# Kernel tuning notes

Hardware: AMD Instinct MI355X
Metric: run time of the kernel (lower is better)

Reference implementation:

```python
import jax, jax.numpy as jnp
import numpy as np

N_SPANS = 4096
EMB_DIM = 384
HEADS = 4
DECAY_LAMBDA = 5.0
THRESHOLD = 0.1
NEG_SLOPE = 0.2  # PyG GATConv default leaky_relu slope


def setup_inputs() -> dict:
    key = jax.random.key(0)
    k1, k2, k3, k4, k5, k6 = jax.random.split(key, 6)
    embeddings = jax.random.normal(k1, (N_SPANS, EMB_DIM), dtype=jnp.float32)
    span_positions = jnp.sort(
        jax.random.randint(k2, (N_SPANS, 2), 0, 100000), axis=1
    ).astype(jnp.int64)
    # GATConv params: lin (no bias), per-head attention vectors, output bias
    glorot = 1.0 / np.sqrt(EMB_DIM)
    W = jax.random.normal(k3, (EMB_DIM, HEADS, EMB_DIM), dtype=jnp.float32) * glorot
    att_src = jax.random.normal(k4, (HEADS, EMB_DIM), dtype=jnp.float32) * glorot
    att_dst = jax.random.normal(k5, (HEADS, EMB_DIM), dtype=jnp.float32) * glorot
    bias = jnp.zeros((EMB_DIM,), dtype=jnp.float32)
    return {
        "embeddings": embeddings,
        "span_positions": span_positions,
        "W": W,
        "att_src": att_src,
        "att_dst": att_dst,
        "bias": bias,
    }


def _adjacency_mask(embeddings):
    # A_ij = cos_sim(e_i, e_j) * exp(-|i - j| / lambda); edges where A > 0.1
    n = embeddings.shape[0]
    en = embeddings / jnp.linalg.norm(embeddings, axis=1, keepdims=True)
    cos_sim = en @ en.T  # [N, N]
    idx = jnp.arange(n, dtype=embeddings.dtype)
    decay = jnp.exp(-jnp.abs(idx[None, :] - idx[:, None]) / DECAY_LAMBDA)
    adj = cos_sim * decay
    # diagonal is 1.0 > threshold, so self-loops (required by GATConv) are present
    return adj > THRESHOLD  # symmetric mask: mask[i, j] == edge j -> i


def reference(embeddings, span_positions, W, att_src, att_dst, bias):
    mask = _adjacency_mask(embeddings)  # [N_dst, N_src]
    # GATConv(heads=4, concat=False): project, per-head additive attention
    x = jnp.einsum("nd,dhe->nhe", embeddings, W)  # [N, H, E]
    a_src = jnp.einsum("nhe,he->nh", x, att_src)  # [N, H]
    a_dst = jnp.einsum("nhe,he->nh", x, att_dst)  # [N, H]
    # logits[i, j, h] for edge j -> i
    logits = jax.nn.leaky_relu(a_dst[:, None, :] + a_src[None, :, :], NEG_SLOPE)
    logits = jnp.where(mask[:, :, None], logits, jnp.float32(-jnp.inf))
    alpha = jax.nn.softmax(logits, axis=1)  # softmax over incoming sources j
    out = jnp.einsum("ijh,jhe->ihe", alpha, x)  # [N, H, E]
    out = out.mean(axis=1) + bias  # concat=False -> mean over heads, then bias
    return out
```

## Files before the change

### kernel.cpp

```cpp
#include <hip/hip_runtime.h>
#include <hip/hip_bf16.h>
#include <math.h>

#define N_SPANS 4096
#define EMB 384
#define HEADS 4
#define HE (HEADS * EMB)
#define BAND 11
#define BW (2 * BAND + 1)

typedef short bf16x8 __attribute__((ext_vector_type(8)));
typedef float f32x4 __attribute__((ext_vector_type(4)));

__device__ __forceinline__ unsigned short f2bf(float f) {
    union { float f; unsigned u; } x; x.f = f;
    unsigned r = x.u + 0x7fffu + ((x.u >> 16) & 1u);
    return (unsigned short)(r >> 16);
}
__device__ __forceinline__ float bf2f(unsigned short u) {
    union { unsigned u; float f; } x; x.u = ((unsigned)u) << 16; return x.f;
}

__device__ __forceinline__ float wave_sum(float v) {
    #pragma unroll
    for (int off = 32; off; off >>= 1) v += __shfl_xor(v, off, 64);
    return v;
}
__device__ __forceinline__ float wave_max(float v) {
    #pragma unroll
    for (int off = 32; off; off >>= 1) v = fmaxf(v, __shfl_xor(v, off, 64));
    return v;
}

__device__ __forceinline__ void gl2lds16(const void* g, void* l) {
    __builtin_amdgcn_global_load_lds(
        (const __attribute__((address_space(1))) void*)(uintptr_t)g,
        (__attribute__((address_space(3))) void*)(unsigned)(uintptr_t)l,
        16, 0, 0);
}

__global__ __launch_bounds__(256) void prep(const float* __restrict__ E,
                                            const float* __restrict__ W,
                                            unsigned short* __restrict__ Ebf,
                                            unsigned short* __restrict__ Wt,
                                            float* __restrict__ invn,
                                            float* __restrict__ attacc) {
    __shared__ float tile[32][33];
    const int b = blockIdx.x;
    const int tid = threadIdx.x;
    if (b < 1024) {
        const int lane = tid & 63, w = tid >> 6;
        const int n = b * 4 + w;
        const float4* er = (const float4*)(E + n * EMB);
        unsigned short* orow = Ebf + n * EMB;
        float s = 0.f;
        float4 v0 = er[lane];
        s += v0.x * v0.x + v0.y * v0.y + v0.z * v0.z + v0.w * v0.w;
        ushort4 c0;
        c0.x = f2bf(v0.x); c0.y = f2bf(v0.y); c0.z = f2bf(v0.z); c0.w = f2bf(v0.w);
        ((ushort4*)orow)[lane] = c0;
        if (lane < 32) {
            float4 v1 = er[lane + 64];
            s += v1.x * v1.x + v1.y * v1.y + v1.z * v1.z + v1.w * v1.w;
            ushort4 c1;
            c1.x = f2bf(v1.x); c1.y = f2bf(v1.y); c1.z = f2bf(v1.z); c1.w = f2bf(v1.w);
            ((ushort4*)orow)[lane + 64] = c1;
        }
        s = wave_sum(s);
        if (lane == 0) invn[n] = 1.0f / sqrtf(s);
    } else if (b < 1600) {
        const int t = b - 1024;
        const int n0 = (t % 48) * 32;
        const int k0 = (t / 48) * 32;
        const int tx = tid & 31, ty = tid >> 5;
        #pragma unroll
        for (int q = 0; q < 4; ++q)
            tile[ty + q * 8][tx] = W[(k0 + ty + q * 8) * HE + n0 + tx];
        __syncthreads();
        #pragma unroll
        for (int q = 0; q < 4; ++q)
            Wt[(n0 + ty + q * 8) * EMB + k0 + tx] = f2bf(tile[tx][ty + q * 8]);
    } else {
        const int t = b - 1600;
        ((float4*)attacc)[t * 256 + tid] = make_float4(0.f, 0.f, 0.f, 0.f);
    }
}

__global__ __launch_bounds__(256) void gemm_attn(const unsigned short* __restrict__ Ebf,
                                                 const unsigned short* __restrict__ Wt,
                                                 const float* __restrict__ attS,
                                                 const float* __restrict__ attD,
                                                 unsigned short* __restrict__ Xb,
                                                 float* __restrict__ asrc,
                                                 float* __restrict__ adst) {
    __shared__ unsigned short As[128 * 32];
    __shared__ unsigned short Bs[128 * 32];
    const int tid = threadIdx.x;
    const int lane = tid & 63;
    const int wave = tid >> 6;
    const int m0 = blockIdx.y * 128;
    const int n0 = blockIdx.x * 128;
    const int wr = (wave >> 1) * 64;
    const int wc = (wave & 1) * 64;
    const int quad = lane >> 4;
    const int l16 = lane & 15;

    const char* Ab = (const char*)Ebf + (size_t)(m0 + wave * 32 + (lane >> 2)) * 768 + (lane & 3) * 16;
    const char* Bb = (const char*)Wt  + (size_t)(n0 + wave * 32 + (lane >> 2)) * 768 + (lane & 3) * 16;
    char* AsB = (char*)As + wave * 32 * 64;
    char* BsB = (char*)Bs + wave * 32 * 64;

    f32x4 acc[4][4];
    #pragma unroll
    for (int i = 0; i < 4; ++i)
        #pragma unroll
        for (int j = 0; j < 4; ++j) acc[i][j] = 0.f;

    for (int kt = 0; kt < 12; ++kt) {
        const int kb = kt * 64;
        __syncthreads();
        gl2lds16(Ab + kb,            AsB);
        gl2lds16(Ab + kb + 16 * 768, AsB + 16 * 64);
        gl2lds16(Bb + kb,            BsB);
        gl2lds16(Bb + kb + 16 * 768, BsB + 16 * 64);
        __syncthreads();

        bf16x8 af[4], bfr[4];
        #pragma unroll
        for (int t = 0; t < 4; ++t) {
            af[t]  = *(const bf16x8*)(&As[(wr + t * 16 + l16) * 32 + quad * 8]);
            bfr[t] = *(const bf16x8*)(&Bs[(wc + t * 16 + l16) * 32 + quad * 8]);
        }
        #pragma unroll
        for (int ti = 0; ti < 4; ++ti)
            #pragma unroll
            for (int tj = 0; tj < 4; ++tj)
                acc[ti][tj] = __builtin_amdgcn_mfma_f32_16x16x32_bf16(
                    af[ti], bfr[tj], acc[ti][tj], 0, 0, 0);
    }

    const int hblk = (n0 + wc) / EMB;
    float aS[4], aD[4];
    #pragma unroll
    for (int tj = 0; tj < 4; ++tj) {
        int col = n0 + wc + tj * 16 + l16;
        aS[tj] = attS[col];
        aD[tj] = attD[col];
    }
    #pragma unroll
    for (int ti = 0; ti < 4; ++ti)
        #pragma unroll
        for (int r = 0; r < 4; ++r) {
            float ps = 0.f, pd = 0.f;
            #pragma unroll
            for (int tj = 0; tj < 4; ++tj) {
                float v = acc[ti][tj][r];
                ps += v * aS[tj];
                pd += v * aD[tj];
            }
            #pragma unroll
            for (int off = 1; off < 16; off <<= 1) {
                ps += __shfl_xor(ps, off, 64);
                pd += __shfl_xor(pd, off, 64);
            }
            if (l16 == 0) {
                int row = m0 + wr + ti * 16 + quad * 4 + r;
                atomicAdd(&asrc[row * HEADS + hblk], ps);
                atomicAdd(&adst[row * HEADS + hblk], pd);
            }
        }

    #pragma unroll
    for (int ti = 0; ti < 4; ++ti)
        #pragma unroll
        for (int tj = 0; tj < 4; ++tj) {
            int col = n0 + wc + tj * 16 + l16;
            #pragma unroll
            for (int r = 0; r < 4; ++r) {
                int row = m0 + wr + ti * 16 + quad * 4 + r;
                Xb[row * HE + col] = f2bf(acc[ti][tj][r]);
            }
        }
}

__global__ __launch_bounds__(256) void band_attn(const float* __restrict__ E,
                                                 const float* __restrict__ invn,
                                                 const float* __restrict__ asrc,
                                                 const float* __restrict__ adst,
                                                 const unsigned short* __restrict__ Xb,
                                                 const float* __restrict__ bias,
                                                 float* __restrict__ out) {
    const int i = blockIdx.x;
    const int tid = threadIdx.x;
    const int lane = tid & 63, wave = tid >> 6;

    __shared__ float ei[EMB];
    __shared__ float alpha_s[HEADS][BW];
    __shared__ int maskv[BW];
    __shared__ int list[BW];
    __shared__ int cnt;

    for (int d = tid; d < EMB; d += 256) ei[d] = E[i * EMB + d];
    __syncthreads();

    const float inv_i = invn[i];
    for (int it = 0; it < 6; ++it) {
        int jo = it * 4 + wave;
        if (jo < BW) {
            int j = i - BAND + jo;
            bool valid = (j >= 0) && (j < N_SPANS);
            float s = 0.f;
            if (valid) {
                const float* ej = E + j * EMB;
                #pragma unroll
                for (int m = 0; m < 6; ++m) {
                    int d = m * 64 + lane;
                    s += ei[d] * ej[d];
                }
                s = wave_sum(s);
            }
            if (lane == 0) {
                int mflag = 0;
                if (valid) {
                    float cosv = s * inv_i * invn[j];
                    int dd = jo - BAND; if (dd < 0) dd = -dd;
                    float a = cosv * expf(-(float)dd * 0.2f);
                    if (a > 0.1f) mflag = 1;
                }
                maskv[jo] = mflag;
            }
        }
    }
    __syncthreads();

    {
        const int h = wave;
        const int jo = lane;
        float logit = -INFINITY;
        if (jo < BW && maskv[jo]) {
            int j = i - BAND + jo;
            float z = adst[i * HEADS + h] + asrc[j * HEADS + h];
            logit = (z >= 0.f) ? z : 0.2f * z;
        }
        float mx = wave_max(logit);
        float ex = (jo < BW) ? expf(logit - mx) : 0.f;
        float sm = wave_sum(ex);
        if (jo < BW) alpha_s[h][jo] = ex / sm;
    }
    __syncthreads();

    if (tid == 0) {
        int c = 0;
        for (int jo = 0; jo < BW; ++jo) if (maskv[jo]) list[c++] = jo;
        cnt = c;
    }
    __syncthreads();

    const int c = cnt;
    for (int e = tid; e < EMB; e += 256) {
        float acc = 0.f;
        for (int ii = 0; ii < c; ++ii) {
            int jo = list[ii];
            int j = i - BAND + jo;
            const unsigned short* xb = Xb + j * HE + e;
            #pragma unroll
            for (int h = 0; h < HEADS; ++h)
                acc += alpha_s[h][jo] * bf2f(xb[h * EMB]);
        }
        out[i * EMB + e] = 0.25f * acc + bias[e];
    }
}

extern "C" void kernel_launch(void* const* d_in, const int* in_sizes, int n_in,
                              void* d_out, int out_size, void* d_ws, size_t ws_size,
                              hipStream_t stream) {
    const float* E       = (const float*)d_in[0];
    const float* W       = (const float*)d_in[2];
    const float* att_src = (const float*)d_in[3];
    const float* att_dst = (const float*)d_in[4];
    const float* bias    = (const float*)d_in[5];
    float* out = (float*)d_out;

    char* ws = (char*)d_ws;
    unsigned short* Xb  = (unsigned short*)ws;
    unsigned short* Ebf = (unsigned short*)(ws + 12582912);
    unsigned short* Wt  = (unsigned short*)(ws + 15728640);
    float* invn         = (float*)(ws + 16908288);
    float* asrc         = (float*)(ws + 16924672);
    float* adst         = (float*)(ws + 16990208);

    prep<<<1632, 256, 0, stream>>>(E, W, Ebf, Wt, invn, asrc );
    gemm_attn<<<dim3(12, 32), 256, 0, stream>>>(Ebf, Wt, att_src, att_dst, Xb, asrc, adst);
    band_attn<<<4096, 256, 0, stream>>>(E, invn, asrc, adst, Xb, bias, out);
}
```

Baseline: 119.0 us.

## Precompute banded dot products in prep and map one wave per row in band_attn

The prep kernel now computes each row's dot products with its next 11 neighbours while it converts the embeddings to bf16, and stores them in a Dots buffer. band_attn then only looks up these symmetric dots instead of re-reading fp32 neighbour rows. band_attn now handles one row per wave, with four rows per block. The mask is built with a ballot and popcount and the softmax runs in registers, so the block-wide syncthreads and the serial list build are gone. In exchange prep makes more neighbour reads, and each row's aggregation now runs on a single wave.

```diff
diff --git a/kernel.cpp b/kernel.cpp
--- a/kernel.cpp
+++ b/kernel.cpp
@@ -44,6 +44,7 @@
                                             unsigned short* __restrict__ Ebf,
                                             unsigned short* __restrict__ Wt,
                                             float* __restrict__ invn,
+                                            float* __restrict__ Dots,
                                             float* __restrict__ attacc) {
     __shared__ float tile[32][33];
     const int b = blockIdx.x;
@@ -51,23 +52,40 @@
     if (b < 1024) {
         const int lane = tid & 63, w = tid >> 6;
         const int n = b * 4 + w;
-        const float4* er = (const float4*)(E + n * EMB);
-        unsigned short* orow = Ebf + n * EMB;
-        float s = 0.f;
-        float4 v0 = er[lane];
-        s += v0.x * v0.x + v0.y * v0.y + v0.z * v0.z + v0.w * v0.w;
-        ushort4 c0;
-        c0.x = f2bf(v0.x); c0.y = f2bf(v0.y); c0.z = f2bf(v0.z); c0.w = f2bf(v0.w);
-        ((ushort4*)orow)[lane] = c0;
-        if (lane < 32) {
-            float4 v1 = er[lane + 64];
-            s += v1.x * v1.x + v1.y * v1.y + v1.z * v1.z + v1.w * v1.w;
-            ushort4 c1;
-            c1.x = f2bf(v1.x); c1.y = f2bf(v1.y); c1.z = f2bf(v1.z); c1.w = f2bf(v1.w);
-            ((ushort4*)orow)[lane + 64] = c1;
-        }
-        s = wave_sum(s);
-        if (lane == 0) invn[n] = 1.0f / sqrtf(s);
+        const float* er = E + (size_t)n * EMB;
+        const int dmax = (n >= N_SPANS - BAND) ? (N_SPANS - 1 - n) : BAND;
+        const float* nb[BAND];
+        #pragma unroll
+        for (int d = 1; d <= BAND; ++d) {
+            int j = n + d; if (j > N_SPANS - 1) j = N_SPANS - 1;
+            nb[d - 1] = E + (size_t)j * EMB;
+        }
+        float acc[12];
+        #pragma unroll
+        for (int d = 0; d < 12; ++d) acc[d] = 0.f;
+        float ev[6];
+        #pragma unroll
+        for (int m = 0; m < 6; ++m) {
+            const int k = m * 64 + lane;
+            const float v = er[k];
+            ev[m] = v;
+            acc[0] += v * v;
+            #pragma unroll
+            for (int d = 1; d <= BAND; ++d) {
+                float u = nb[d - 1][k];
+                acc[d] += (d <= dmax) ? v * u : 0.f;
+            }
+        }
+        #pragma unroll
+        for (int m = 0; m < 6; ++m)
+            Ebf[(size_t)n * EMB + m * 64 + lane] = f2bf(ev[m]);
+        #pragma unroll
+        for (int d = 0; d < 12; ++d) acc[d] = wave_sum(acc[d]);
+        float dval = 0.f;
+        #pragma unroll
+        for (int d = 1; d <= BAND; ++d) if (lane == d) dval = acc[d];
+        if (lane >= 1 && lane <= BAND) Dots[(size_t)n * 12 + lane] = dval;
+        if (lane == 0) invn[n] = 1.0f / sqrtf(acc[0]);
     } else if (b < 1600) {
         const int t = b - 1024;
         const int n0 = (t % 48) * 32;
@@ -183,89 +201,67 @@
         }
 }
 
-__global__ __launch_bounds__(256) void band_attn(const float* __restrict__ E,
-                                                 const float* __restrict__ invn,
+__global__ __launch_bounds__(256) void band_attn(const float* __restrict__ invn,
+                                                 const float* __restrict__ Dots,
                                                  const float* __restrict__ asrc,
                                                  const float* __restrict__ adst,
                                                  const unsigned short* __restrict__ Xb,
                                                  const float* __restrict__ bias,
                                                  float* __restrict__ out) {
-    const int i = blockIdx.x;
-    const int tid = threadIdx.x;
-    const int lane = tid & 63, wave = tid >> 6;
-
-    __shared__ float ei[EMB];
-    __shared__ float alpha_s[HEADS][BW];
-    __shared__ int maskv[BW];
-    __shared__ int list[BW];
-    __shared__ int cnt;
-
-    for (int d = tid; d < EMB; d += 256) ei[d] = E[i * EMB + d];
-    __syncthreads();
-
-    const float inv_i = invn[i];
-    for (int it = 0; it < 6; ++it) {
-        int jo = it * 4 + wave;
-        if (jo < BW) {
-            int j = i - BAND + jo;
-            bool valid = (j >= 0) && (j < N_SPANS);
-            float s = 0.f;
-            if (valid) {
-                const float* ej = E + j * EMB;
-                #pragma unroll
-                for (int m = 0; m < 6; ++m) {
-                    int d = m * 64 + lane;
-                    s += ei[d] * ej[d];
-                }
-                s = wave_sum(s);
-            }
-            if (lane == 0) {
-                int mflag = 0;
-                if (valid) {
-                    float cosv = s * inv_i * invn[j];
-                    int dd = jo - BAND; if (dd < 0) dd = -dd;
-                    float a = cosv * expf(-(float)dd * 0.2f);
-                    if (a > 0.1f) mflag = 1;
-                }
-                maskv[jo] = mflag;
-            }
-        }
-    }
-    __syncthreads();
-
-    {
-        const int h = wave;
-        const int jo = lane;
-        float logit = -INFINITY;
-        if (jo < BW && maskv[jo]) {
-            int j = i - BAND + jo;
-            float z = adst[i * HEADS + h] + asrc[j * HEADS + h];
-            logit = (z >= 0.f) ? z : 0.2f * z;
-        }
-        float mx = wave_max(logit);
-        float ex = (jo < BW) ? expf(logit - mx) : 0.f;
+    __shared__ float sAl[4][BW][4];
+    __shared__ int sList[4][24];
+    const int tid = threadIdx.x, lane = tid & 63, w = tid >> 6;
+    const int i = blockIdx.x * 4 + w;
+    const int jo = lane;
+    const int j = i - BAND + jo;
+    const bool inb = (jo < BW) && (j >= 0) && (j < N_SPANS);
+    const int jc = inb ? j : i;
+
+    float dotv = 0.f;
+    if (inb) {
+        if (jo < BAND)      dotv = Dots[(size_t)j * 12 + (BAND - jo)];
+        else if (jo > BAND) dotv = Dots[(size_t)i * 12 + (jo - BAND)];
+    }
+    bool flag;
+    if (jo == BAND) {
+        flag = true;
+    } else {
+        int dd = jo < BAND ? BAND - jo : jo - BAND;
+        float a = ((dotv * invn[i]) * invn[jc]) * expf(-(float)dd * 0.2f);
+        flag = inb && (a > 0.1f);
+    }
+
+    unsigned long long mbits = __ballot(flag);
+    const int cnt = __popcll(mbits);
+    const int rank = __popcll(mbits & ((1ull << jo) - 1ull));
+    if (flag) sList[w][rank] = jo;
+
+    const float4 ad = ((const float4*)adst)[i];
+    const float4 as = inb ? ((const float4*)asrc)[jc] : make_float4(0.f, 0.f, 0.f, 0.f);
+    float al[4];
+    #pragma unroll
+    for (int h = 0; h < 4; ++h) {
+        float z = (&ad.x)[h] + (&as.x)[h];
+        z = (z >= 0.f) ? z : 0.2f * z;
+        float lg = flag ? z : -INFINITY;
+        float mx = wave_max(lg);
+        float ex = flag ? expf(lg - mx) : 0.f;
         float sm = wave_sum(ex);
-        if (jo < BW) alpha_s[h][jo] = ex / sm;
-    }
-    __syncthreads();
-
-    if (tid == 0) {
-        int c = 0;
-        for (int jo = 0; jo < BW; ++jo) if (maskv[jo]) list[c++] = jo;
-        cnt = c;
-    }
-    __syncthreads();
-
-    const int c = cnt;
-    for (int e = tid; e < EMB; e += 256) {
+        al[h] = ex / sm;
+    }
+    if (flag) *(float4*)&sAl[w][jo][0] = make_float4(al[0], al[1], al[2], al[3]);
+
+    #pragma unroll
+    for (int m = 0; m < 6; ++m) {
+        const int e = m * 64 + lane;
         float acc = 0.f;
-        for (int ii = 0; ii < c; ++ii) {
-            int jo = list[ii];
-            int j = i - BAND + jo;
-            const unsigned short* xb = Xb + j * HE + e;
-            #pragma unroll
-            for (int h = 0; h < HEADS; ++h)
-                acc += alpha_s[h][jo] * bf2f(xb[h * EMB]);
+        for (int ii = 0; ii < cnt; ++ii) {
+            const int joL = sList[w][ii];
+            const int jj = i - BAND + joL;
+            const float4 a4 = *(const float4*)&sAl[w][joL][0];
+            const unsigned short* xr = Xb + (size_t)jj * HE + e;
+            acc += a4.x * bf2f(xr[0])   + a4.y * bf2f(xr[384])
+                 + a4.z * bf2f(xr[768]) + a4.w * bf2f(xr[1152]);
         }
         out[i * EMB + e] = 0.25f * acc + bias[e];
     }
@@ -288,8 +284,9 @@
     float* invn         = (float*)(ws + 16908288);
     float* asrc         = (float*)(ws + 16924672);
     float* adst         = (float*)(ws + 16990208);
-
-    prep<<<1632, 256, 0, stream>>>(E, W, Ebf, Wt, invn, asrc );
+    float* Dots         = (float*)(ws + 17055744);
+
+    prep<<<1632, 256, 0, stream>>>(E, W, Ebf, Wt, invn, Dots, asrc );
     gemm_attn<<<dim3(12, 32), 256, 0, stream>>>(Ebf, Wt, att_src, att_dst, Xb, asrc, adst);
-    band_attn<<<4096, 256, 0, stream>>>(E, invn, asrc, adst, Xb, bias, out);
-}
+    band_attn<<<1024, 256, 0, stream>>>(invn, Dots, asrc, adst, Xb, bias, out);
+}
```

Result: faster. 109.6 us (-7.9%).
